# Kernel tuning notes

Measured on AMD Instinct MI355X. Metric: run time of the kernel, lower is better.

Reference implementation:

```python
import jax, jax.numpy as jnp
import numpy as np

B, N, C, H, P = 4, 8192, 256, 4, 64  # batch, tokens(=input_size), hidden, heads, proj_size
D = C // H


def setup_inputs() -> dict:
    key = jax.random.key(0)
    ks = jax.random.split(key, 12)
    s = 1.0 / np.sqrt(C)
    inp = {
        "x": jax.random.normal(ks[0], (B, N, C), jnp.float32),
        "q": jax.random.normal(ks[1], (B, N, C), jnp.float32),
        "Wq": jax.random.normal(ks[2], (C, C), jnp.float32) * s,
        "Wk": jax.random.normal(ks[3], (C, C), jnp.float32) * s,
        "Wv_ca": jax.random.normal(ks[4], (C, C), jnp.float32) * s,
        "Wv_sa": jax.random.normal(ks[5], (C, C), jnp.float32) * s,
        "E_w": jax.random.normal(ks[6], (P, N), jnp.float32) * (1.0 / np.sqrt(N)),
        "E_b": jnp.zeros((P,), jnp.float32),
        "temp": jnp.ones((H, 1, 1), jnp.float32),
        "temp2": jnp.ones((H, 1, 1), jnp.float32),
        "Wo1": jax.random.normal(ks[7], (C // 2, C), jnp.float32) * s,
        "bo1": jnp.zeros((C // 2,), jnp.float32),
        "Wo2": jax.random.normal(ks[8], (C // 2, C), jnp.float32) * s,
        "bo2": jnp.zeros((C // 2,), jnp.float32),
    }
    return inp


def _l2norm(t):
    # F.normalize(dim=-1): x / max(||x||_2, 1e-12)
    n = jnp.sqrt(jnp.sum(t * t, axis=-1, keepdims=True))
    return t / jnp.maximum(n, 1e-12)


def reference(x, q, Wq, Wk, Wv_ca, Wv_sa, E_w, E_b, temp, temp2, Wo1, bo1, Wo2, bo2):
    b, n, c = x.shape
    h, d = H, c // H

    def split(t):  # [B,N,C] -> [B,H,d,N]
        return t.reshape(b, n, h, d).transpose(0, 2, 3, 1)

    qs = split(q @ Wq.T)
    ks = split(x @ Wk.T)
    v_ca = split(x @ Wv_ca.T)
    v_sa = split(x @ Wv_sa.T)

    # Linformer-style projections E (=F) over token dim N -> P
    k_proj = jnp.einsum('bhdn,pn->bhdp', ks, E_w) + E_b   # [B,H,d,P]
    v_proj = jnp.einsum('bhdn,pn->bhdp', v_sa, E_w) + E_b  # [B,H,d,P]

    qn = _l2norm(qs)
    kn = _l2norm(ks)

    # Channel attention: [B,H,d,d]
    attn_ca = jax.nn.softmax(jnp.einsum('bhdn,bhen->bhde', qn, kn) * temp, axis=-1)
    x_ca = jnp.einsum('bhde,bhen->bhdn', attn_ca, v_ca)
    x_ca = x_ca.transpose(0, 3, 1, 2).reshape(b, n, c)

    # Spatial (projected) attention: [B,H,N,P]
    attn_sa = jax.nn.softmax(jnp.einsum('bhdn,bhdp->bhnp', qn, k_proj) * temp2, axis=-1)
    x_sa = jnp.einsum('bhnp,bhdp->bhnd', attn_sa, v_proj)
    # faithful to original permute(0,3,1,2).reshape(B,N,C)
    x_sa = x_sa.transpose(0, 3, 1, 2).reshape(b, n, c)

    x_sa = x_sa @ Wo1.T + bo1
    x_ca = x_ca @ Wo2.T + bo2
    return jnp.concatenate((x_sa, x_ca), axis=-1)
```

## Files before the change

### kernel.cpp

```cpp
#include <hip/hip_runtime.h>
#include <hip/hip_bf16.h>

#define NN 8192
#define BNC 8388608

typedef unsigned short u16;
typedef unsigned int u32;
typedef __attribute__((ext_vector_type(8))) short bf16x8;
typedef __attribute__((ext_vector_type(4))) float f32x4;
typedef __attribute__((ext_vector_type(4))) float float4v;

__device__ __forceinline__ float bf2f(u16 u) {
    union { u32 i; float f; } c; c.i = ((u32)u) << 16; return c.f;
}
__device__ __forceinline__ u16 f2bf(float f) {
    union { float f; u32 i; } c; c.f = f;
    u32 x = c.i;
    u32 r = (x + 0x7fffu + ((x >> 16) & 1u)) >> 16;
    return (u16)r;
}
__device__ __forceinline__ void gl16(const u16* g, u16* l) {
    __builtin_amdgcn_global_load_lds(
        (const __attribute__((address_space(1))) void*)g,
        (__attribute__((address_space(3))) void*)l, 16, 0, 0);
}

__global__ void fill_kernel(float* __restrict__ out, float val) {
    int base = (blockIdx.x * 256 + threadIdx.x) * 4;
    #pragma unroll
    for (int i = 0; i < 4; ++i) out[base + i] = val;
}

__global__ void zeroconv_kernel(const float* __restrict__ x,
                                const float* __restrict__ Wq, const float* __restrict__ Wk,
                                const float* __restrict__ Wo1, const float* __restrict__ Ew,
                                u16* __restrict__ xb,
                                u16* __restrict__ Wqb, u16* __restrict__ Wkb,
                                u16* __restrict__ Wo1b, u16* __restrict__ Ewb,
                                float* __restrict__ zbase) {
    if (blockIdx.x >= 4432) {
        int i = (blockIdx.x - 4432) * 256 + threadIdx.x;
        if (i < 67584) zbase[i] = 0.f;
        return;
    }
    size_t e = ((size_t)blockIdx.x * 256 + threadIdx.x) * 8;
    const float* src; u16* dst;
    if (e < 8388608)      { src = x   + e;             dst = xb   + e; }
    else if (e < 8454144) { src = Wq  + (e - 8388608); dst = Wqb  + (e - 8388608); }
    else if (e < 8519680) { src = Wk  + (e - 8454144); dst = Wkb  + (e - 8454144); }
    else if (e < 8552448) { src = Wo1 + (e - 8519680); dst = Wo1b + (e - 8519680); }
    else                  { src = Ew  + (e - 8552448); dst = Ewb  + (e - 8552448); }
    float4v f0 = *(const float4v*)src, f1 = *(const float4v*)(src + 4);
    bf16x8 v;
    #pragma unroll
    for (int j = 0; j < 4; ++j) {
        v[j] = (short)f2bf(f0[j]); v[4 + j] = (short)f2bf(f1[j]);
    }
    *(bf16x8*)dst = v;
}

__global__ __launch_bounds__(256) void gemm_qkf(
    const float* __restrict__ qf, const u16* __restrict__ xb,
    const u16* __restrict__ Wqb, const u16* __restrict__ Wkb,
    u16* __restrict__ Qb, u16* __restrict__ Kb,
    float* __restrict__ nq2, float* __restrict__ nk2)
{
    __shared__ u16 As[4096];
    __shared__ u16 Bs[4096];
    const int z = blockIdx.z;
    const u16* Bt = z ? Wkb : Wqb;
    u16* O = z ? Kb : Qb;
    float* dstn = z ? nk2 : nq2;
    const int t = threadIdx.x, lane = t & 63, w = t >> 6;
    const int wr = w >> 1, wc = w & 1;
    const int fr = lane & 15, fk = (lane >> 4) * 8, r0 = (lane >> 4) * 4;
    const int m0 = blockIdx.x * 128, n0 = blockIdx.y * 128;
    const int b = m0 >> 13;
    const int row0 = t >> 2, k80 = (t & 3) * 8;
    const int row1 = (256 + t) >> 2, k81 = ((256 + t) & 3) * 8;

    f32x4 acc[4][4];
    #pragma unroll
    for (int i = 0; i < 4; ++i)
        #pragma unroll
        for (int j = 0; j < 4; ++j) acc[i][j] = (f32x4){0.f, 0.f, 0.f, 0.f};

    for (int kt = 0; kt < 8; ++kt) {
        const int k0 = kt * 32;
        if (z == 0) {
            const float* p0 = qf + (size_t)(m0 + row0) * 256 + k0 + k80;
            float4v f0 = *(const float4v*)p0, f1 = *(const float4v*)(p0 + 4);
            bf16x8 va;
            #pragma unroll
            for (int j = 0; j < 4; ++j) {
                va[j] = (short)f2bf(f0[j]); va[4 + j] = (short)f2bf(f1[j]);
            }
            *(bf16x8*)&As[t * 8] = va;
            const float* p1 = qf + (size_t)(m0 + row1) * 256 + k0 + k81;
            float4v g0 = *(const float4v*)p1, g1 = *(const float4v*)(p1 + 4);
            bf16x8 vb2;
            #pragma unroll
            for (int j = 0; j < 4; ++j) {
                vb2[j] = (short)f2bf(g0[j]); vb2[4 + j] = (short)f2bf(g1[j]);
            }
            *(bf16x8*)&As[(256 + t) * 8] = vb2;
        } else {
            gl16(xb + (size_t)(m0 + row0) * 256 + k0 + k80, &As[t * 8]);
            gl16(xb + (size_t)(m0 + row1) * 256 + k0 + k81, &As[(256 + t) * 8]);
        }
        gl16(Bt + (size_t)(n0 + row0) * 256 + k0 + k80, &Bs[t * 8]);
        gl16(Bt + (size_t)(n0 + row1) * 256 + k0 + k81, &Bs[(256 + t) * 8]);
        __syncthreads();
        bf16x8 a[4], bfr[4];
        #pragma unroll
        for (int fm = 0; fm < 4; ++fm)
            a[fm] = *(const bf16x8*)&As[(wr * 64 + fm * 16 + fr) * 32 + fk];
        #pragma unroll
        for (int fn = 0; fn < 4; ++fn)
            bfr[fn] = *(const bf16x8*)&Bs[(wc * 64 + fn * 16 + fr) * 32 + fk];
        #pragma unroll
        for (int fm = 0; fm < 4; ++fm)
            #pragma unroll
            for (int fn = 0; fn < 4; ++fn)
                acc[fm][fn] = __builtin_amdgcn_mfma_f32_16x16x32_bf16(
                    a[fm], bfr[fn], acc[fm][fn], 0, 0, 0);
        __syncthreads();
    }

    #pragma unroll
    for (int fn = 0; fn < 4; ++fn) {
        int gcol = n0 + wc * 64 + fn * 16 + fr;
        float s = 0.f;
        #pragma unroll
        for (int fm = 0; fm < 4; ++fm) {
            #pragma unroll
            for (int r = 0; r < 4; ++r) {
                size_t grow = (size_t)(m0 + wr * 64 + fm * 16 + r0 + r);
                float v = acc[fm][fn][r];
                O[grow * 256 + gcol] = f2bf(v);
                s += v * v;
            }
        }
        s += __shfl_xor(s, 16);
        s += __shfl_xor(s, 32);
        if (lane < 16) atomicAdd(&dstn[b * 256 + gcol], s);
    }
}

__global__ __launch_bounds__(256) void xecalog_kernel(
    const u16* __restrict__ xb, const u16* __restrict__ Ewb, float* __restrict__ xE,
    const u16* __restrict__ Qb, const u16* __restrict__ Kb, float* __restrict__ cpart)
{
    __shared__ u16 smA[64][136];
    __shared__ u16 smB[64][136];
    const int t = threadIdx.x, lane = t & 63, w = t >> 6;
    const int fr = lane & 15, fk = (lane >> 4) * 8, r0 = (lane >> 4) * 4;

    f32x4 acc[4][4];
    #pragma unroll
    for (int i = 0; i < 4; ++i)
        #pragma unroll
        for (int j = 0; j < 4; ++j) acc[i][j] = (f32x4){0.f, 0.f, 0.f, 0.f};

    if (blockIdx.x < 256) {
        const int bkq = blockIdx.x >> 4, nc = blockIdx.x & 15;
        const int b = bkq >> 2, kq = bkq & 3;
        for (int it = 0; it < 4; ++it) {
            const int n0 = nc * 512 + it * 128;
            #pragma unroll
            for (int i = 0; i < 4; ++i) {
                int c = i * 256 + t, tok = c >> 3, kl = (c & 7) * 8;
                const int sw = tok ^ ((kl >> 3) << 3);
                bf16x8 v = *(const bf16x8*)(xb + ((size_t)b * NN + n0 + tok) * 256 + kq * 64 + kl);
                #pragma unroll
                for (int j = 0; j < 8; ++j) smA[kl + j][sw] = (u16)v[j];
            }
            #pragma unroll
            for (int i = 0; i < 4; ++i) {
                int c = i * 256 + t, p = c >> 4, tk8 = (c & 15) * 8;
                *(bf16x8*)&smB[p][tk8] = *(const bf16x8*)(Ewb + (size_t)p * NN + n0 + tk8);
            }
            __syncthreads();
            bf16x8 a[4], bb[4];
            #pragma unroll
            for (int fm = 0; fm < 4; ++fm) {
                int row = fm * 16 + fr;
                a[fm] = *(const bf16x8*)&smA[row][(w * 32 + fk) ^ (((row >> 3) & 7) << 3)];
            }
            #pragma unroll
            for (int fn = 0; fn < 4; ++fn)
                bb[fn] = *(const bf16x8*)&smB[fn * 16 + fr][w * 32 + fk];
            #pragma unroll
            for (int fm = 0; fm < 4; ++fm)
                #pragma unroll
                for (int fn = 0; fn < 4; ++fn)
                    acc[fm][fn] = __builtin_amdgcn_mfma_f32_16x16x32_bf16(
                        a[fm], bb[fn], acc[fm][fn], 0, 0, 0);
            __syncthreads();
        }
        float* Cred = (float*)&smA[0][0];
        for (int ph = 0; ph < 4; ++ph) {
            if (w == ph) {
                #pragma unroll
                for (int fm = 0; fm < 4; ++fm)
                    #pragma unroll
                    for (int fn = 0; fn < 4; ++fn)
                        #pragma unroll
                        for (int r = 0; r < 4; ++r) {
                            int idx = (fm * 16 + r0 + r) * 64 + fn * 16 + fr;
                            if (ph == 0) Cred[idx] = acc[fm][fn][r];
                            else         Cred[idx] += acc[fm][fn][r];
                        }
            }
            __syncthreads();
        }
        float* dst = xE + (size_t)(b * 256 + kq * 64) * 64;
        #pragma unroll
        for (int i = 0; i < 16; ++i) atomicAdd(&dst[i * 256 + t], Cred[i * 256 + t]);
    } else {
        const int bx = blockIdx.x - 256;
        const int bh = bx >> 4, nc = bx & 15;
        const int b = bh >> 2, h = bh & 3;
        for (int it = 0; it < 4; ++it) {
            const int n0 = nc * 512 + it * 128;
            #pragma unroll
            for (int i = 0; i < 4; ++i) {
                int c = i * 256 + t, tok = c >> 3, ch8 = (c & 7) * 8;
                const int sw = tok ^ ((ch8 >> 3) << 3);
                size_t g = ((size_t)b * NN + n0 + tok) * 256 + h * 64 + ch8;
                bf16x8 vq = *(const bf16x8*)(Qb + g);
                bf16x8 vk = *(const bf16x8*)(Kb + g);
                #pragma unroll
                for (int j = 0; j < 8; ++j) {
                    smA[ch8 + j][sw] = (u16)vq[j];
                    smB[ch8 + j][sw] = (u16)vk[j];
                }
            }
            __syncthreads();
            bf16x8 a[4], bb[4];
            #pragma unroll
            for (int fm = 0; fm < 4; ++fm) {
                int row = fm * 16 + fr;
                a[fm] = *(const bf16x8*)&smA[row][(w * 32 + fk) ^ (((row >> 3) & 7) << 3)];
            }
            #pragma unroll
            for (int fn = 0; fn < 4; ++fn) {
                int row = fn * 16 + fr;
                bb[fn] = *(const bf16x8*)&smB[row][(w * 32 + fk) ^ (((row >> 3) & 7) << 3)];
            }
            #pragma unroll
            for (int fm = 0; fm < 4; ++fm)
                #pragma unroll
                for (int fn = 0; fn < 4; ++fn)
                    acc[fm][fn] = __builtin_amdgcn_mfma_f32_16x16x32_bf16(
                        a[fm], bb[fn], acc[fm][fn], 0, 0, 0);
            __syncthreads();
        }
        float* Cred = (float*)&smA[0][0];
        for (int ph = 0; ph < 4; ++ph) {
            if (w == ph) {
                #pragma unroll
                for (int fm = 0; fm < 4; ++fm)
                    #pragma unroll
                    for (int fn = 0; fn < 4; ++fn)
                        #pragma unroll
                        for (int r = 0; r < 4; ++r) {
                            int idx = (fm * 16 + r0 + r) * 64 + fn * 16 + fr;
                            if (ph == 0) Cred[idx] = acc[fm][fn][r];
                            else         Cred[idx] += acc[fm][fn][r];
                        }
            }
            __syncthreads();
        }
        float* dst = cpart + (size_t)nc * 65536 + (size_t)bh * 4096;
        #pragma unroll
        for (int i = 0; i < 16; ++i) dst[i * 256 + t] = Cred[i * 256 + t];
    }
}

__global__ __launch_bounds__(256) void smkv_kernel(
    const float* __restrict__ cpart, const float* __restrict__ nq2,
    const float* __restrict__ nk2, const float* __restrict__ temp,
    float* __restrict__ caprob,
    const float* __restrict__ Wk, const float* __restrict__ Wvsa,
    const float* __restrict__ xE, const float* __restrict__ Eb,
    float* __restrict__ kp, float* __restrict__ vp) {
    const int t = threadIdx.x;
    if (blockIdx.x < 256) {
        const int row = blockIdx.x * 4 + (t >> 6);
        const int e = t & 63;
        const int b = row >> 8, c = row & 255, h = c >> 6;
        const int i = row * 64 + e;
        float lg = cpart[i];
        #pragma unroll
        for (int nc = 1; nc < 16; ++nc) lg += cpart[(size_t)nc * 65536 + i];
        float nq = fmaxf(sqrtf(nq2[row]), 1e-12f);
        float nk = fmaxf(sqrtf(nk2[b * 256 + h * 64 + e]), 1e-12f);
        float v = lg / (nq * nk) * temp[h];
        float m = v;
        #pragma unroll
        for (int o = 32; o; o >>= 1) m = fmaxf(m, __shfl_xor(m, o));
        float ex = __expf(v - m);
        float s = ex;
        #pragma unroll
        for (int o = 32; o; o >>= 1) s += __shfl_xor(s, o);
        caprob[i] = ex / s;
    } else {
        const int idx = blockIdx.x - 256;
        const int z = idx >> 8, bc4 = idx & 255;
        const int b = bc4 >> 6, c = (bc4 & 63) * 4 + (t >> 6);
        const int p = t & 63;
        const float* W = z ? Wvsa : Wk;
        float* dst = z ? vp : kp;
        float s = 0.f;
        for (int k = 0; k < 256; ++k)
            s += W[c * 256 + k] * xE[(size_t)(b * 256 + k) * 64 + p];
        dst[(size_t)(b * 256 + c) * 64 + p] = s + Eb[p];
    }
}

__global__ __launch_bounds__(256) void samw_kernel(
    const u16* __restrict__ Qb, const float* __restrict__ kp,
    const float* __restrict__ vp, const float* __restrict__ nq2,
    const float* __restrict__ temp2, u16* __restrict__ xsa,
    const float* __restrict__ caprob, const float* __restrict__ Wo2,
    const float* __restrict__ Wvca, u16* __restrict__ W2effb)
{
    __shared__ char smem[49152];
    const int t = threadIdx.x;
    if (blockIdx.x >= 512) {
        float* Ml = (float*)smem;
        const int bj = blockIdx.x - 512;
        const int b = bj >> 7, j = bj & 127;
        const int h = t >> 6, e = t & 63;
        float s = 0.f;
        #pragma unroll 8
        for (int d = 0; d < 64; ++d)
            s += Wo2[j * 256 + h * 64 + d] * caprob[(size_t)(b * 256 + h * 64 + d) * 64 + e];
        Ml[t] = s;
        __syncthreads();
        float s2 = 0.f;
        for (int c = 0; c < 256; ++c) s2 += Ml[c] * Wvca[c * 256 + t];
        W2effb[(size_t)bj * 256 + t] = f2bf(s2);
        return;
    }
    u16* Qs = (u16*)smem;
    u16* KT = (u16*)(smem + 32768);
    u16* VT = (u16*)(smem + 40960);
    const int nc = blockIdx.x & 31, bh = blockIdx.x >> 5, b = bh >> 2, h = bh & 3;
    const int lane = t & 63, w = t >> 6;
    const int fr = lane & 15, fk = (lane >> 4) * 8, r0 = (lane >> 4) * 4;

    #pragma unroll
    for (int i = 0; i < 8; ++i) {
        int c = i * 256 + t, tok = c >> 3, ch8 = (c & 7) * 8;
        *(bf16x8*)&Qs[c * 8] =
            *(const bf16x8*)(Qb + ((size_t)b * NN + nc * 256 + tok) * 256 + h * 64 + ch8);
    }
    {
        const int d = t >> 2, p0 = (t & 3) * 16;
        const float rqv = 1.0f / fmaxf(sqrtf(nq2[b * 256 + h * 64 + d]), 1e-12f);
        const float t2 = temp2[h];
        const float* kr = kp + (size_t)(b * 256 + h * 64 + d) * 64 + p0;
        #pragma unroll
        for (int j = 0; j < 16; ++j)
            KT[(p0 + j) * 64 + d] = f2bf(kr[j] * rqv * t2);
    }
    {
        const float* vs = vp + (size_t)(b * 256 + h * 64) * 64;
        #pragma unroll
        for (int i = 0; i < 2; ++i) {
            int c = i * 256 + t;
            bf16x8 v;
            #pragma unroll
            for (int j = 0; j < 8; ++j) v[j] = (short)f2bf(vs[c * 8 + j]);
            *(bf16x8*)&VT[c * 8] = v;
        }
    }
    __syncthreads();

    f32x4 acc[4][4];
    #pragma unroll
    for (int i = 0; i < 4; ++i)
        #pragma unroll
        for (int j = 0; j < 4; ++j) acc[i][j] = (f32x4){0.f, 0.f, 0.f, 0.f};
    #pragma unroll
    for (int ks = 0; ks < 2; ++ks) {
        bf16x8 a[4], bb[4];
        #pragma unroll
        for (int fm = 0; fm < 4; ++fm)
            a[fm] = *(const bf16x8*)&Qs[(w * 64 + fm * 16 + fr) * 64 + ks * 32 + fk];
        #pragma unroll
        for (int fn = 0; fn < 4; ++fn)
            bb[fn] = *(const bf16x8*)&KT[(fn * 16 + fr) * 64 + ks * 32 + fk];
        #pragma unroll
        for (int fm = 0; fm < 4; ++fm)
            #pragma unroll
            for (int fn = 0; fn < 4; ++fn)
                acc[fm][fn] = __builtin_amdgcn_mfma_f32_16x16x32_bf16(
                    a[fm], bb[fn], acc[fm][fn], 0, 0, 0);
    }
    __syncthreads();

    u16* Pw = Qs + w * 4096;
    #pragma unroll
    for (int fm = 0; fm < 4; ++fm) {
        #pragma unroll
        for (int r = 0; r < 4; ++r) {
            float m = fmaxf(fmaxf(acc[fm][0][r], acc[fm][1][r]),
                            fmaxf(acc[fm][2][r], acc[fm][3][r]));
            m = fmaxf(m, __shfl_xor(m, 1));
            m = fmaxf(m, __shfl_xor(m, 2));
            m = fmaxf(m, __shfl_xor(m, 4));
            m = fmaxf(m, __shfl_xor(m, 8));
            float e0 = __expf(acc[fm][0][r] - m), e1 = __expf(acc[fm][1][r] - m);
            float e2 = __expf(acc[fm][2][r] - m), e3 = __expf(acc[fm][3][r] - m);
            float s = e0 + e1 + e2 + e3;
            s += __shfl_xor(s, 1); s += __shfl_xor(s, 2);
            s += __shfl_xor(s, 4); s += __shfl_xor(s, 8);
            float rs = 1.0f / s;
            int row = fm * 16 + r0 + r;
            Pw[row * 64 +  0 + fr] = f2bf(e0 * rs);
            Pw[row * 64 + 16 + fr] = f2bf(e1 * rs);
            Pw[row * 64 + 32 + fr] = f2bf(e2 * rs);
            Pw[row * 64 + 48 + fr] = f2bf(e3 * rs);
        }
    }

    f32x4 acc2[4][4];
    #pragma unroll
    for (int i = 0; i < 4; ++i)
        #pragma unroll
        for (int j = 0; j < 4; ++j) acc2[i][j] = (f32x4){0.f, 0.f, 0.f, 0.f};
    #pragma unroll
    for (int ks = 0; ks < 2; ++ks) {
        bf16x8 a[4], bb[4];
        #pragma unroll
        for (int fm = 0; fm < 4; ++fm)
            a[fm] = *(const bf16x8*)&Pw[(fm * 16 + fr) * 64 + ks * 32 + fk];
        #pragma unroll
        for (int fn = 0; fn < 4; ++fn)
            bb[fn] = *(const bf16x8*)&VT[(fn * 16 + fr) * 64 + ks * 32 + fk];
        #pragma unroll
        for (int fm = 0; fm < 4; ++fm)
            #pragma unroll
            for (int fn = 0; fn < 4; ++fn)
                acc2[fm][fn] = __builtin_amdgcn_mfma_f32_16x16x32_bf16(
                    a[fm], bb[fn], acc2[fm][fn], 0, 0, 0);
    }
    __syncthreads();

    u16* X2 = Qs;
    #pragma unroll
    for (int fm = 0; fm < 4; ++fm)
        #pragma unroll
        for (int fn = 0; fn < 4; ++fn)
            #pragma unroll
            for (int r = 0; r < 4; ++r)
                X2[(w * 64 + fm * 16 + r0 + r) * 64 + fn * 16 + fr] = f2bf(acc2[fm][fn][r]);
    __syncthreads();

    {
        const int d = t >> 2, cq = (t & 3) * 64;
        u16* orow = xsa + ((size_t)b * NN + d * 128 + h * 32 + nc) * 256 + cq;
        #pragma unroll
        for (int i = 0; i < 8; ++i) {
            bf16x8 v;
            #pragma unroll
            for (int j = 0; j < 8; ++j) v[j] = (short)X2[(cq + i * 8 + j) * 64 + d];
            *(bf16x8*)&orow[i * 8] = v;
        }
    }
}

__global__ __launch_bounds__(256) void outgemm(
    const u16* __restrict__ xsa, const u16* __restrict__ xb,
    const u16* __restrict__ Wo1b, const u16* __restrict__ W2effb,
    const float* __restrict__ bo1, const float* __restrict__ bo2,
    float* __restrict__ out)
{
    __shared__ u16 As[4096];
    __shared__ u16 Bs[4096];
    const int z = blockIdx.z;
    const u16* A = z ? xb : xsa;
    const u16* Bt = z ? (W2effb + (size_t)(blockIdx.x >> 6) * 128 * 256) : Wo1b;
    const float* bias = z ? bo2 : bo1;
    const int outoff = z ? 128 : 0;
    const int t = threadIdx.x, lane = t & 63, w = t >> 6;
    const int wr = w >> 1, wc = w & 1;
    const int fr = lane & 15, fk = (lane >> 4) * 8, r0 = (lane >> 4) * 4;
    const int m0 = blockIdx.x * 128;
    const int row0 = t >> 2, k80 = (t & 3) * 8;
    const int row1 = (256 + t) >> 2, k81 = ((256 + t) & 3) * 8;

    f32x4 acc[4][4];
    #pragma unroll
    for (int i = 0; i < 4; ++i)
        #pragma unroll
        for (int j = 0; j < 4; ++j) acc[i][j] = (f32x4){0.f, 0.f, 0.f, 0.f};

    for (int kt = 0; kt < 8; ++kt) {
        const int k0 = kt * 32;
        gl16(A  + (size_t)(m0 + row0) * 256 + k0 + k80, &As[t * 8]);
        gl16(A  + (size_t)(m0 + row1) * 256 + k0 + k81, &As[(256 + t) * 8]);
        gl16(Bt + (size_t)row0 * 256 + k0 + k80, &Bs[t * 8]);
        gl16(Bt + (size_t)row1 * 256 + k0 + k81, &Bs[(256 + t) * 8]);
        __syncthreads();
        bf16x8 a[4], bfr[4];
        #pragma unroll
        for (int fm = 0; fm < 4; ++fm)
            a[fm] = *(const bf16x8*)&As[(wr * 64 + fm * 16 + fr) * 32 + fk];
        #pragma unroll
        for (int fn = 0; fn < 4; ++fn)
            bfr[fn] = *(const bf16x8*)&Bs[(wc * 64 + fn * 16 + fr) * 32 + fk];
        #pragma unroll
        for (int fm = 0; fm < 4; ++fm)
            #pragma unroll
            for (int fn = 0; fn < 4; ++fn)
                acc[fm][fn] = __builtin_amdgcn_mfma_f32_16x16x32_bf16(
                    a[fm], bfr[fn], acc[fm][fn], 0, 0, 0);
        __syncthreads();
    }

    #pragma unroll
    for (int fm = 0; fm < 4; ++fm)
        #pragma unroll
        for (int fn = 0; fn < 4; ++fn) {
            int gcol = wc * 64 + fn * 16 + fr;
            #pragma unroll
            for (int r = 0; r < 4; ++r) {
                size_t grow = (size_t)(m0 + wr * 64 + fm * 16 + r0 + r);
                out[grow * 256 + outoff + gcol] = acc[fm][fn][r] + bias[gcol];
            }
        }
}

extern "C" void kernel_launch(void* const* d_in, const int* in_sizes, int n_in,
                              void* d_out, int out_size, void* d_ws, size_t ws_size,
                              hipStream_t stream) {
    float* out = (float*)d_out;

    static const int expect[14] = {8388608, 8388608, 65536, 65536, 65536, 65536,
                                   524288, 64, 4, 4, 32768, 128, 32768, 128};
    bool ok = (n_in == 14) && (out_size == 8388608);
    if (ok) for (int i = 0; i < 14; ++i) ok = ok && (in_sizes[i] == expect[i]);
    if (!ok) {
        fill_kernel<<<dim3(8192), 256, 0, stream>>>(out, 3000.0f);
        return;
    }
    if (ws_size < 80000000u) {
        fill_kernel<<<dim3(8192), 256, 0, stream>>>(out, 1000.0f);
        return;
    }

    const float* x    = (const float*)d_in[0];
    const float* q    = (const float*)d_in[1];
    const float* Wq   = (const float*)d_in[2];
    const float* Wk   = (const float*)d_in[3];
    const float* Wvca = (const float*)d_in[4];
    const float* Wvsa = (const float*)d_in[5];
    const float* Ew   = (const float*)d_in[6];
    const float* Eb   = (const float*)d_in[7];
    const float* temp = (const float*)d_in[8];
    const float* temp2= (const float*)d_in[9];
    const float* Wo1  = (const float*)d_in[10];
    const float* bo1  = (const float*)d_in[11];
    const float* Wo2  = (const float*)d_in[12];
    const float* bo2  = (const float*)d_in[13];

    u16* Qb   = (u16*)d_ws;
    u16* Kb   = Qb + (size_t)BNC;
    u16* xb   = Kb + (size_t)BNC;
    u16* Wqb  = xb + (size_t)BNC;
    u16* Wkb  = Wqb + 65536;
    u16* Wo1b = Wkb + 65536;
    u16* Ewb  = Wo1b + 32768;
    u16* W2effb = Ewb + 524288;
    u16* xsa  = Kb;
    float* fs    = (float*)(W2effb + 131072);
    float* nq2   = fs;
    float* nk2   = nq2 + 1024;
    float* xE    = nk2 + 1024;
    float* kp    = xE + 65536;
    float* vp    = kp + 65536;
    float* caprob= vp + 65536;
    float* cpart = caprob + 65536;

    zeroconv_kernel<<<dim3(4696), 256, 0, stream>>>(x, Wq, Wk, Wo1, Ew,
                                                    xb, Wqb, Wkb, Wo1b, Ewb, nq2);
    gemm_qkf<<<dim3(256, 2, 2), 256, 0, stream>>>(q, xb, Wqb, Wkb, Qb, Kb, nq2, nk2);
    xecalog_kernel<<<dim3(512), 256, 0, stream>>>(xb, Ewb, xE, Qb, Kb, cpart);
    smkv_kernel<<<dim3(768), 256, 0, stream>>>(cpart, nq2, nk2, temp, caprob,
                                               Wk, Wvsa, xE, Eb, kp, vp);
    samw_kernel<<<dim3(1024), 256, 0, stream>>>(Qb, kp, vp, nq2, temp2, xsa,
                                                caprob, Wo2, Wvca, W2effb);
    outgemm<<<dim3(256, 1, 2), 256, 0, stream>>>(xsa, xb, Wo1b, W2effb, bo1, bo2, out);
}
```

Measured before the change: 105.8 us.

## Regroup kernel stages so independent work shares launches by dependency

Kernel boundaries are reshuffled along the dependency graph. The Q/K GEMM now shares a launch with the x·E projection, the channel logits share one with the kp/vp projection, the channel softmax shares one with spatial attention, the W2eff build shares one with the Wo1 output GEMM, and the channel output GEMM runs alone at the end. The aim is to fill the GPU with independent blocks and cut the tail idle time in each stage. The risks are that the fused kernels take the larger shared-memory footprint, which may lower occupancy, and that the kernel count stays the same.

Result: no change. 105.5 us, median of 2 (-0.3%).

```diff
diff --git a/kernel.cpp b/kernel.cpp
--- a/kernel.cpp
+++ b/kernel.cpp
@@ -59,112 +59,109 @@
     *(bf16x8*)dst = v;
 }
 
-__global__ __launch_bounds__(256) void gemm_qkf(
+__global__ __launch_bounds__(256) void qkxe_kernel(
     const float* __restrict__ qf, const u16* __restrict__ xb,
     const u16* __restrict__ Wqb, const u16* __restrict__ Wkb,
     u16* __restrict__ Qb, u16* __restrict__ Kb,
-    float* __restrict__ nq2, float* __restrict__ nk2)
+    float* __restrict__ nq2, float* __restrict__ nk2,
+    const u16* __restrict__ Ewb, float* __restrict__ xE)
 {
-    __shared__ u16 As[4096];
-    __shared__ u16 Bs[4096];
-    const int z = blockIdx.z;
-    const u16* Bt = z ? Wkb : Wqb;
-    u16* O = z ? Kb : Qb;
-    float* dstn = z ? nk2 : nq2;
-    const int t = threadIdx.x, lane = t & 63, w = t >> 6;
-    const int wr = w >> 1, wc = w & 1;
-    const int fr = lane & 15, fk = (lane >> 4) * 8, r0 = (lane >> 4) * 4;
-    const int m0 = blockIdx.x * 128, n0 = blockIdx.y * 128;
-    const int b = m0 >> 13;
-    const int row0 = t >> 2, k80 = (t & 3) * 8;
-    const int row1 = (256 + t) >> 2, k81 = ((256 + t) & 3) * 8;
-
-    f32x4 acc[4][4];
-    #pragma unroll
-    for (int i = 0; i < 4; ++i)
-        #pragma unroll
-        for (int j = 0; j < 4; ++j) acc[i][j] = (f32x4){0.f, 0.f, 0.f, 0.f};
-
-    for (int kt = 0; kt < 8; ++kt) {
-        const int k0 = kt * 32;
-        if (z == 0) {
-            const float* p0 = qf + (size_t)(m0 + row0) * 256 + k0 + k80;
-            float4v f0 = *(const float4v*)p0, f1 = *(const float4v*)(p0 + 4);
-            bf16x8 va;
-            #pragma unroll
-            for (int j = 0; j < 4; ++j) {
-                va[j] = (short)f2bf(f0[j]); va[4 + j] = (short)f2bf(f1[j]);
-            }
-            *(bf16x8*)&As[t * 8] = va;
-            const float* p1 = qf + (size_t)(m0 + row1) * 256 + k0 + k81;
-            float4v g0 = *(const float4v*)p1, g1 = *(const float4v*)(p1 + 4);
-            bf16x8 vb2;
-            #pragma unroll
-            for (int j = 0; j < 4; ++j) {
-                vb2[j] = (short)f2bf(g0[j]); vb2[4 + j] = (short)f2bf(g1[j]);
-            }
-            *(bf16x8*)&As[(256 + t) * 8] = vb2;
-        } else {
-            gl16(xb + (size_t)(m0 + row0) * 256 + k0 + k80, &As[t * 8]);
-            gl16(xb + (size_t)(m0 + row1) * 256 + k0 + k81, &As[(256 + t) * 8]);
-        }
-        gl16(Bt + (size_t)(n0 + row0) * 256 + k0 + k80, &Bs[t * 8]);
-        gl16(Bt + (size_t)(n0 + row1) * 256 + k0 + k81, &Bs[(256 + t) * 8]);
-        __syncthreads();
-        bf16x8 a[4], bfr[4];
-        #pragma unroll
-        for (int fm = 0; fm < 4; ++fm)
-            a[fm] = *(const bf16x8*)&As[(wr * 64 + fm * 16 + fr) * 32 + fk];
-        #pragma unroll
-        for (int fn = 0; fn < 4; ++fn)
-            bfr[fn] = *(const bf16x8*)&Bs[(wc * 64 + fn * 16 + fr) * 32 + fk];
-        #pragma unroll
-        for (int fm = 0; fm < 4; ++fm)
-            #pragma unroll
-            for (int fn = 0; fn < 4; ++fn)
-                acc[fm][fn] = __builtin_amdgcn_mfma_f32_16x16x32_bf16(
-                    a[fm], bfr[fn], acc[fm][fn], 0, 0, 0);
-        __syncthreads();
-    }
-
-    #pragma unroll
-    for (int fn = 0; fn < 4; ++fn) {
-        int gcol = n0 + wc * 64 + fn * 16 + fr;
-        float s = 0.f;
-        #pragma unroll
-        for (int fm = 0; fm < 4; ++fm) {
-            #pragma unroll
-            for (int r = 0; r < 4; ++r) {
-                size_t grow = (size_t)(m0 + wr * 64 + fm * 16 + r0 + r);
-                float v = acc[fm][fn][r];
-                O[grow * 256 + gcol] = f2bf(v);
-                s += v * v;
-            }
-        }
-        s += __shfl_xor(s, 16);
-        s += __shfl_xor(s, 32);
-        if (lane < 16) atomicAdd(&dstn[b * 256 + gcol], s);
-    }
-}
-
-__global__ __launch_bounds__(256) void xecalog_kernel(
-    const u16* __restrict__ xb, const u16* __restrict__ Ewb, float* __restrict__ xE,
-    const u16* __restrict__ Qb, const u16* __restrict__ Kb, float* __restrict__ cpart)
-{
-    __shared__ u16 smA[64][136];
-    __shared__ u16 smB[64][136];
+    __shared__ u16 sm[17408];
     const int t = threadIdx.x, lane = t & 63, w = t >> 6;
     const int fr = lane & 15, fk = (lane >> 4) * 8, r0 = (lane >> 4) * 4;
 
-    f32x4 acc[4][4];
-    #pragma unroll
-    for (int i = 0; i < 4; ++i)
-        #pragma unroll
-        for (int j = 0; j < 4; ++j) acc[i][j] = (f32x4){0.f, 0.f, 0.f, 0.f};
-
-    if (blockIdx.x < 256) {
-        const int bkq = blockIdx.x >> 4, nc = blockIdx.x & 15;
+    if (blockIdx.x < 1024) {
+        u16* As = sm;
+        u16* Bs = sm + 4096;
+        const int mt = blockIdx.x & 255, nt = (blockIdx.x >> 8) & 1, z = blockIdx.x >> 9;
+        const u16* Bt = z ? Wkb : Wqb;
+        u16* O = z ? Kb : Qb;
+        float* dstn = z ? nk2 : nq2;
+        const int wr = w >> 1, wc = w & 1;
+        const int m0 = mt * 128, n0 = nt * 128;
+        const int b = m0 >> 13;
+        const int row0 = t >> 2, k80 = (t & 3) * 8;
+        const int row1 = (256 + t) >> 2, k81 = ((256 + t) & 3) * 8;
+
+        f32x4 acc[4][4];
+        #pragma unroll
+        for (int i = 0; i < 4; ++i)
+            #pragma unroll
+            for (int j = 0; j < 4; ++j) acc[i][j] = (f32x4){0.f, 0.f, 0.f, 0.f};
+
+        for (int kt = 0; kt < 8; ++kt) {
+            const int k0 = kt * 32;
+            if (z == 0) {
+                const float* p0 = qf + (size_t)(m0 + row0) * 256 + k0 + k80;
+                float4v f0 = *(const float4v*)p0, f1 = *(const float4v*)(p0 + 4);
+                bf16x8 va;
+                #pragma unroll
+                for (int j = 0; j < 4; ++j) {
+                    va[j] = (short)f2bf(f0[j]); va[4 + j] = (short)f2bf(f1[j]);
+                }
+                *(bf16x8*)&As[t * 8] = va;
+                const float* p1 = qf + (size_t)(m0 + row1) * 256 + k0 + k81;
+                float4v g0 = *(const float4v*)p1, g1 = *(const float4v*)(p1 + 4);
+                bf16x8 vb2;
+                #pragma unroll
+                for (int j = 0; j < 4; ++j) {
+                    vb2[j] = (short)f2bf(g0[j]); vb2[4 + j] = (short)f2bf(g1[j]);
+                }
+                *(bf16x8*)&As[(256 + t) * 8] = vb2;
+            } else {
+                gl16(xb + (size_t)(m0 + row0) * 256 + k0 + k80, &As[t * 8]);
+                gl16(xb + (size_t)(m0 + row1) * 256 + k0 + k81, &As[(256 + t) * 8]);
+            }
+            gl16(Bt + (size_t)(n0 + row0) * 256 + k0 + k80, &Bs[t * 8]);
+            gl16(Bt + (size_t)(n0 + row1) * 256 + k0 + k81, &Bs[(256 + t) * 8]);
+            __syncthreads();
+            bf16x8 a[4], bfr[4];
+            #pragma unroll
+            for (int fm = 0; fm < 4; ++fm)
+                a[fm] = *(const bf16x8*)&As[(wr * 64 + fm * 16 + fr) * 32 + fk];
+            #pragma unroll
+            for (int fn = 0; fn < 4; ++fn)
+                bfr[fn] = *(const bf16x8*)&Bs[(wc * 64 + fn * 16 + fr) * 32 + fk];
+            #pragma unroll
+            for (int fm = 0; fm < 4; ++fm)
+                #pragma unroll
+                for (int fn = 0; fn < 4; ++fn)
+                    acc[fm][fn] = __builtin_amdgcn_mfma_f32_16x16x32_bf16(
+                        a[fm], bfr[fn], acc[fm][fn], 0, 0, 0);
+            __syncthreads();
+        }
+
+        #pragma unroll
+        for (int fn = 0; fn < 4; ++fn) {
+            int gcol = n0 + wc * 64 + fn * 16 + fr;
+            float s = 0.f;
+            #pragma unroll
+            for (int fm = 0; fm < 4; ++fm) {
+                #pragma unroll
+                for (int r = 0; r < 4; ++r) {
+                    size_t grow = (size_t)(m0 + wr * 64 + fm * 16 + r0 + r);
+                    float v = acc[fm][fn][r];
+                    O[grow * 256 + gcol] = f2bf(v);
+                    s += v * v;
+                }
+            }
+            s += __shfl_xor(s, 16);
+            s += __shfl_xor(s, 32);
+            if (lane < 16) atomicAdd(&dstn[b * 256 + gcol], s);
+        }
+    } else {
+        u16 (*smA)[136] = (u16(*)[136])sm;
+        u16 (*smB)[136] = (u16(*)[136])(sm + 8704);
+        const int bx2 = blockIdx.x - 1024;
+        const int bkq = bx2 >> 4, nc = bx2 & 15;
         const int b = bkq >> 2, kq = bkq & 3;
+
+        f32x4 acc[4][4];
+        #pragma unroll
+        for (int i = 0; i < 4; ++i)
+            #pragma unroll
+            for (int j = 0; j < 4; ++j) acc[i][j] = (f32x4){0.f, 0.f, 0.f, 0.f};
+
         for (int it = 0; it < 4; ++it) {
             const int n0 = nc * 512 + it * 128;
             #pragma unroll
@@ -217,10 +214,31 @@
         float* dst = xE + (size_t)(b * 256 + kq * 64) * 64;
         #pragma unroll
         for (int i = 0; i < 16; ++i) atomicAdd(&dst[i * 256 + t], Cred[i * 256 + t]);
-    } else {
-        const int bx = blockIdx.x - 256;
-        const int bh = bx >> 4, nc = bx & 15;
+    }
+}
+
+__global__ __launch_bounds__(256) void calogkv_kernel(
+    const u16* __restrict__ Qb, const u16* __restrict__ Kb, float* __restrict__ cpart,
+    const float* __restrict__ Wk, const float* __restrict__ Wvsa,
+    const float* __restrict__ xE, const float* __restrict__ Eb,
+    float* __restrict__ kp, float* __restrict__ vp)
+{
+    __shared__ u16 sm[17408];
+    const int t = threadIdx.x, lane = t & 63, w = t >> 6;
+    const int fr = lane & 15, fk = (lane >> 4) * 8, r0 = (lane >> 4) * 4;
+
+    if (blockIdx.x < 256) {
+        u16 (*smA)[136] = (u16(*)[136])sm;
+        u16 (*smB)[136] = (u16(*)[136])(sm + 8704);
+        const int bh = blockIdx.x >> 4, nc = blockIdx.x & 15;
         const int b = bh >> 2, h = bh & 3;
+
+        f32x4 acc[4][4];
+        #pragma unroll
+        for (int i = 0; i < 4; ++i)
+            #pragma unroll
+            for (int j = 0; j < 4; ++j) acc[i][j] = (f32x4){0.f, 0.f, 0.f, 0.f};
+
         for (int it = 0; it < 4; ++it) {
             const int n0 = nc * 512 + it * 128;
             #pragma unroll
@@ -275,36 +293,6 @@
         float* dst = cpart + (size_t)nc * 65536 + (size_t)bh * 4096;
         #pragma unroll
         for (int i = 0; i < 16; ++i) dst[i * 256 + t] = Cred[i * 256 + t];
-    }
-}
-
-__global__ __launch_bounds__(256) void smkv_kernel(
-    const float* __restrict__ cpart, const float* __restrict__ nq2,
-    const float* __restrict__ nk2, const float* __restrict__ temp,
-    float* __restrict__ caprob,
-    const float* __restrict__ Wk, const float* __restrict__ Wvsa,
-    const float* __restrict__ xE, const float* __restrict__ Eb,
-    float* __restrict__ kp, float* __restrict__ vp) {
-    const int t = threadIdx.x;
-    if (blockIdx.x < 256) {
-        const int row = blockIdx.x * 4 + (t >> 6);
-        const int e = t & 63;
-        const int b = row >> 8, c = row & 255, h = c >> 6;
-        const int i = row * 64 + e;
-        float lg = cpart[i];
-        #pragma unroll
-        for (int nc = 1; nc < 16; ++nc) lg += cpart[(size_t)nc * 65536 + i];
-        float nq = fmaxf(sqrtf(nq2[row]), 1e-12f);
-        float nk = fmaxf(sqrtf(nk2[b * 256 + h * 64 + e]), 1e-12f);
-        float v = lg / (nq * nk) * temp[h];
-        float m = v;
-        #pragma unroll
-        for (int o = 32; o; o >>= 1) m = fmaxf(m, __shfl_xor(m, o));
-        float ex = __expf(v - m);
-        float s = ex;
-        #pragma unroll
-        for (int o = 32; o; o >>= 1) s += __shfl_xor(s, o);
-        caprob[i] = ex / s;
     } else {
         const int idx = blockIdx.x - 256;
         const int z = idx >> 8, bc4 = idx & 255;
@@ -319,35 +307,42 @@
     }
 }
 
-__global__ __launch_bounds__(256) void samw_kernel(
+__global__ __launch_bounds__(256) void smsa_kernel(
+    const float* __restrict__ cpart, const float* __restrict__ nq2,
+    const float* __restrict__ nk2, const float* __restrict__ temp,
+    float* __restrict__ caprob,
     const u16* __restrict__ Qb, const float* __restrict__ kp,
-    const float* __restrict__ vp, const float* __restrict__ nq2,
-    const float* __restrict__ temp2, u16* __restrict__ xsa,
-    const float* __restrict__ caprob, const float* __restrict__ Wo2,
-    const float* __restrict__ Wvca, u16* __restrict__ W2effb)
+    const float* __restrict__ vp, const float* __restrict__ temp2,
+    u16* __restrict__ xsa)
 {
     __shared__ char smem[49152];
     const int t = threadIdx.x;
-    if (blockIdx.x >= 512) {
-        float* Ml = (float*)smem;
-        const int bj = blockIdx.x - 512;
-        const int b = bj >> 7, j = bj & 127;
-        const int h = t >> 6, e = t & 63;
-        float s = 0.f;
-        #pragma unroll 8
-        for (int d = 0; d < 64; ++d)
-            s += Wo2[j * 256 + h * 64 + d] * caprob[(size_t)(b * 256 + h * 64 + d) * 64 + e];
-        Ml[t] = s;
-        __syncthreads();
-        float s2 = 0.f;
-        for (int c = 0; c < 256; ++c) s2 += Ml[c] * Wvca[c * 256 + t];
-        W2effb[(size_t)bj * 256 + t] = f2bf(s2);
+    if (blockIdx.x < 256) {
+        const int row = blockIdx.x * 4 + (t >> 6);
+        const int e = t & 63;
+        const int b = row >> 8, c = row & 255, h = c >> 6;
+        const int i = row * 64 + e;
+        float lg = cpart[i];
+        #pragma unroll
+        for (int nc = 1; nc < 16; ++nc) lg += cpart[(size_t)nc * 65536 + i];
+        float nq = fmaxf(sqrtf(nq2[row]), 1e-12f);
+        float nk = fmaxf(sqrtf(nk2[b * 256 + h * 64 + e]), 1e-12f);
+        float v = lg / (nq * nk) * temp[h];
+        float m = v;
+        #pragma unroll
+        for (int o = 32; o; o >>= 1) m = fmaxf(m, __shfl_xor(m, o));
+        float ex = __expf(v - m);
+        float s = ex;
+        #pragma unroll
+        for (int o = 32; o; o >>= 1) s += __shfl_xor(s, o);
+        caprob[i] = ex / s;
         return;
     }
     u16* Qs = (u16*)smem;
     u16* KT = (u16*)(smem + 32768);
     u16* VT = (u16*)(smem + 40960);
-    const int nc = blockIdx.x & 31, bh = blockIdx.x >> 5, b = bh >> 2, h = bh & 3;
+    const int bx2 = blockIdx.x - 256;
+    const int nc = bx2 & 31, bh = bx2 >> 5, b = bh >> 2, h = bh & 3;
     const int lane = t & 63, w = t >> 6;
     const int fr = lane & 15, fk = (lane >> 4) * 8, r0 = (lane >> 4) * 4;
 
@@ -473,23 +468,14 @@
     }
 }
 
-__global__ __launch_bounds__(256) void outgemm(
-    const u16* __restrict__ xsa, const u16* __restrict__ xb,
-    const u16* __restrict__ Wo1b, const u16* __restrict__ W2effb,
-    const float* __restrict__ bo1, const float* __restrict__ bo2,
-    float* __restrict__ out)
+__device__ __forceinline__ void out_gemm_body(
+    const u16* __restrict__ A, const u16* __restrict__ Bt,
+    const float* __restrict__ bias, int outoff, int m0,
+    float* __restrict__ out, u16* As, u16* Bs, int t)
 {
-    __shared__ u16 As[4096];
-    __shared__ u16 Bs[4096];
-    const int z = blockIdx.z;
-    const u16* A = z ? xb : xsa;
-    const u16* Bt = z ? (W2effb + (size_t)(blockIdx.x >> 6) * 128 * 256) : Wo1b;
-    const float* bias = z ? bo2 : bo1;
-    const int outoff = z ? 128 : 0;
-    const int t = threadIdx.x, lane = t & 63, w = t >> 6;
+    const int lane = t & 63, w = t >> 6;
     const int wr = w >> 1, wc = w & 1;
     const int fr = lane & 15, fk = (lane >> 4) * 8, r0 = (lane >> 4) * 4;
-    const int m0 = blockIdx.x * 128;
     const int row0 = t >> 2, k80 = (t & 3) * 8;
     const int row1 = (256 + t) >> 2, k81 = ((256 + t) & 3) * 8;
 
@@ -533,6 +519,45 @@
                 out[grow * 256 + outoff + gcol] = acc[fm][fn][r] + bias[gcol];
             }
         }
+}
+
+__global__ __launch_bounds__(256) void mwout_kernel(
+    const float* __restrict__ caprob, const float* __restrict__ Wo2,
+    const float* __restrict__ Wvca, u16* __restrict__ W2effb,
+    const u16* __restrict__ xsa, const u16* __restrict__ Wo1b,
+    const float* __restrict__ bo1, float* __restrict__ out)
+{
+    __shared__ u16 sm[8192];
+    const int t = threadIdx.x;
+    if (blockIdx.x < 512) {
+        float* Ml = (float*)sm;
+        const int bj = blockIdx.x;
+        const int b = bj >> 7, j = bj & 127;
+        const int h = t >> 6, e = t & 63;
+        float s = 0.f;
+        #pragma unroll 8
+        for (int d = 0; d < 64; ++d)
+            s += Wo2[j * 256 + h * 64 + d] * caprob[(size_t)(b * 256 + h * 64 + d) * 64 + e];
+        Ml[t] = s;
+        __syncthreads();
+        float s2 = 0.f;
+        for (int c = 0; c < 256; ++c) s2 += Ml[c] * Wvca[c * 256 + t];
+        W2effb[(size_t)bj * 256 + t] = f2bf(s2);
+        return;
+    }
+    const int m0 = (blockIdx.x - 512) * 128;
+    out_gemm_body(xsa, Wo1b, bo1, 0, m0, out, sm, sm + 4096, t);
+}
+
+__global__ __launch_bounds__(256) void outca_kernel(
+    const u16* __restrict__ xb, const u16* __restrict__ W2effb,
+    const float* __restrict__ bo2, float* __restrict__ out)
+{
+    __shared__ u16 sm[8192];
+    const int t = threadIdx.x;
+    const int m0 = blockIdx.x * 128;
+    const u16* Bt = W2effb + (size_t)(blockIdx.x >> 6) * 128 * 256;
+    out_gemm_body(xb, Bt, bo2, 128, m0, out, sm, sm + 4096, t);
 }
 
 extern "C" void kernel_launch(void* const* d_in, const int* in_sizes, int n_in,
@@ -588,11 +613,12 @@
 
     zeroconv_kernel<<<dim3(4696), 256, 0, stream>>>(x, Wq, Wk, Wo1, Ew,
                                                     xb, Wqb, Wkb, Wo1b, Ewb, nq2);
-    gemm_qkf<<<dim3(256, 2, 2), 256, 0, stream>>>(q, xb, Wqb, Wkb, Qb, Kb, nq2, nk2);
-    xecalog_kernel<<<dim3(512), 256, 0, stream>>>(xb, Ewb, xE, Qb, Kb, cpart);
-    smkv_kernel<<<dim3(768), 256, 0, stream>>>(cpart, nq2, nk2, temp, caprob,
-                                               Wk, Wvsa, xE, Eb, kp, vp);
-    samw_kernel<<<dim3(1024), 256, 0, stream>>>(Qb, kp, vp, nq2, temp2, xsa,
-                                                caprob, Wo2, Wvca, W2effb);
-    outgemm<<<dim3(256, 1, 2), 256, 0, stream>>>(xsa, xb, Wo1b, W2effb, bo1, bo2, out);
-}
+    qkxe_kernel<<<dim3(1280), 256, 0, stream>>>(q, xb, Wqb, Wkb, Qb, Kb, nq2, nk2,
+                                                Ewb, xE);
+    calogkv_kernel<<<dim3(768), 256, 0, stream>>>(Qb, Kb, cpart, Wk, Wvsa, xE, Eb, kp, vp);
+    smsa_kernel<<<dim3(768), 256, 0, stream>>>(cpart, nq2, nk2, temp, caprob,
+                                               Qb, kp, vp, temp2, xsa);
+    mwout_kernel<<<dim3(768), 256, 0, stream>>>(caprob, Wo2, Wvca, W2effb,
+                                                xsa, Wo1b, bo1, out);
+    outca_kernel<<<dim3(256), 256, 0, stream>>>(xb, W2effb, bo2, out);
+}
```
